# Optimization experiments

Hardware: AMD Instinct MI355X
Metric: run time of the kernel (lower is better)

Reference implementation:

```python
import jax, jax.numpy as jnp
import numpy as np

N = 50000
E = 1600000
F_IN = 128
C_OUT = 64
HEADS = 2
NEG_SLOPE = 0.2
EPS = 1e-5


def setup_inputs() -> dict:
    key = jax.random.key(0)
    ks = jax.random.split(key, 8)
    HC = HEADS * C_OUT
    glorot = lambda k, shape: jax.random.normal(k, shape, jnp.float32) * np.sqrt(2.0 / (shape[0] + shape[-1]))
    return {
        "x": jax.random.normal(ks[0], (N, F_IN), jnp.float32),
        "edge_index": jax.random.randint(ks[1], (2, E), 0, N, jnp.int64),
        "W_l": glorot(ks[2], (F_IN, HC)),
        "W_r": glorot(ks[3], (F_IN, HC)),
        "att": glorot(ks[4], (HEADS, C_OUT)),
        "bias": jnp.zeros((HC,), jnp.float32),
        "gn_weight": jnp.ones((HC,), jnp.float32),
        "gn_bias": jnp.zeros((HC,), jnp.float32),
        "gn_mean_scale": jnp.ones((HC,), jnp.float32),
    }


def reference(x, edge_index, W_l, W_r, att, bias, gn_weight, gn_bias, gn_mean_scale):
    n = x.shape[0]
    # --- GATv2Conv (share_weights=False, concat=True, dropout=0) ---
    x_l = (x @ W_l).reshape(n, HEADS, C_OUT)  # source transform
    x_r = (x @ W_r).reshape(n, HEADS, C_OUT)  # target transform
    # add self loops
    loop = jnp.arange(n, dtype=edge_index.dtype)
    src = jnp.concatenate([edge_index[0], loop])
    dst = jnp.concatenate([edge_index[1], loop])
    # edge-wise attention logits: LeakyReLU(x_l[j] + x_r[i]) . att
    xs = x_l[src] + x_r[dst]  # [E', H, C]
    e = jax.nn.leaky_relu(xs, NEG_SLOPE)
    logits = jnp.einsum('ehc,hc->eh', e, att)  # [E', H]
    # segment softmax over edges sharing the same target node
    seg_max = jax.ops.segment_max(logits, dst, num_segments=n)  # [N, H]
    exp = jnp.exp(logits - seg_max[dst])
    seg_sum = jax.ops.segment_sum(exp, dst, num_segments=n)
    alpha = exp / seg_sum[dst]  # [E', H]
    # scatter-aggregate messages
    msg = alpha[:, :, None] * x_l[src]  # [E', H, C]
    out = jax.ops.segment_sum(msg, dst, num_segments=n)  # [N, H, C]
    out = out.reshape(n, HEADS * C_OUT) + bias
    # --- GraphNorm (single graph) ---
    mean = out.mean(axis=0)
    centered = out - mean * gn_mean_scale
    var = (centered * centered).mean(axis=0)
    return gn_weight * centered / jnp.sqrt(var + EPS) + gn_bias
```

## Files before the change

kernel.cpp:

```cpp
#include <hip/hip_runtime.h>
#include <math.h>

#define NEG_SLOPE 0.2f
#define GN_EPS 1e-5f
#define NBSHIFT 8
#define CHUNK 2048

typedef _Float16 h2 __attribute__((ext_vector_type(2)));
typedef _Float16 half8 __attribute__((ext_vector_type(8)));
typedef float f32x4 __attribute__((ext_vector_type(4)));

__device__ __forceinline__ int rfl(int v) {
  return __builtin_amdgcn_readfirstlane(v);
}

__device__ __forceinline__ unsigned int pkh(float a, float b) {
  return __builtin_bit_cast(unsigned int, __builtin_amdgcn_cvt_pkrtz(a, b));
}

__device__ __forceinline__ h2 bch2(unsigned int u) {
  return __builtin_bit_cast(h2, u);
}

__device__ __forceinline__ h2 mkh2(float a, float b) {
  return __builtin_bit_cast(h2, __builtin_amdgcn_cvt_pkrtz(a, b));
}

__device__ __forceinline__ float dot2f(h2 a, h2 b, float c) {
#if __has_builtin(__builtin_amdgcn_fdot2)
  return __builtin_amdgcn_fdot2(a, b, c, false);
#else
  return fmaf((float)a.x, (float)b.x, fmaf((float)a.y, (float)b.y, c));
#endif
}

__device__ __forceinline__ float lkdot(h2 xl, h2 xr, h2 a, float p) {
  h2 t = xl + xr;
  h2 z = {(_Float16)0.f, (_Float16)0.f};
#if __has_builtin(__builtin_elementwise_min)
  h2 mn = __builtin_elementwise_min(t, z);
#else
  h2 mn;
  mn.x = (t.x < z.x) ? t.x : z.x;
  mn.y = (t.y < z.y) ? t.y : z.y;
#endif
  h2 km1 = {(_Float16)(NEG_SLOPE - 1.0f), (_Float16)(NEG_SLOPE - 1.0f)};
  h2 g = mn * km1 + t;
  return dot2f(g, a, p);
}

__global__ __launch_bounds__(256) void gemm_hist(
    const float* __restrict__ x, const float* __restrict__ Wl,
    const float* __restrict__ Wr, unsigned int* __restrict__ xlb,
    unsigned int* __restrict__ xrh, int n, const int* __restrict__ ei,
    int* __restrict__ bhist, int e, int gemm_blocks) {
  if ((int)blockIdx.x >= gemm_blocks) {
    __shared__ int hist[256];
    hist[threadIdx.x] = 0;
    __syncthreads();
    const int nbk = gridDim.x - gemm_blocks;
    const int stride = nbk * 256;
    for (int i = ((int)blockIdx.x - gemm_blocks) * 256 + threadIdx.x; i < e;
         i += stride)
      atomicAdd(&hist[ei[e + i] >> NBSHIFT], 1);
    __syncthreads();
    int v = hist[threadIdx.x];
    if (v > 0) atomicAdd(&bhist[threadIdx.x], v);
    return;
  }

  const int wv = threadIdx.x >> 6;
  const int lane = threadIdx.x & 63;
  const int lr = lane & 15;
  const int lk = lane >> 4;
  const int node0 = (int)blockIdx.x * 64;
  const float* __restrict__ Wp = (wv < 2) ? Wl : Wr;
  unsigned int* __restrict__ dst = (wv < 2) ? xlb : xrh;
  const int chBase = (wv & 1) * 64;

  f32x4 acc[4][4];
#pragma unroll
  for (int mt = 0; mt < 4; ++mt)
#pragma unroll
    for (int nt = 0; nt < 4; ++nt) acc[mt][nt] = (f32x4){0.f, 0.f, 0.f, 0.f};

  int nd[4];
#pragma unroll
  for (int nt = 0; nt < 4; ++nt) nd[nt] = min(node0 + nt * 16 + lr, n - 1);

#pragma unroll
  for (int kc = 0; kc < 4; ++kc) {
    const int k0 = kc * 32 + lk * 8;
    half8 a[4];
#pragma unroll
    for (int mt = 0; mt < 4; ++mt) {
      const float* __restrict__ wp =
          Wp + (size_t)k0 * 128 + chBase + mt * 16 + lr;
      float w0 = wp[0 * 128], w1 = wp[1 * 128], w2 = wp[2 * 128],
            w3 = wp[3 * 128];
      float w4 = wp[4 * 128], w5 = wp[5 * 128], w6 = wp[6 * 128],
            w7 = wp[7 * 128];
      uint4 ua;
      ua.x = pkh(w0, w1);
      ua.y = pkh(w2, w3);
      ua.z = pkh(w4, w5);
      ua.w = pkh(w6, w7);
      a[mt] = __builtin_bit_cast(half8, ua);
    }
    half8 b[4];
#pragma unroll
    for (int nt = 0; nt < 4; ++nt) {
      const float4 f0 = *(const float4*)(x + (size_t)nd[nt] * 128 + k0);
      const float4 f1 = *(const float4*)(x + (size_t)nd[nt] * 128 + k0 + 4);
      uint4 ub;
      ub.x = pkh(f0.x, f0.y);
      ub.y = pkh(f0.z, f0.w);
      ub.z = pkh(f1.x, f1.y);
      ub.w = pkh(f1.z, f1.w);
      b[nt] = __builtin_bit_cast(half8, ub);
    }
#pragma unroll
    for (int mt = 0; mt < 4; ++mt)
#pragma unroll
      for (int nt = 0; nt < 4; ++nt)
        acc[mt][nt] = __builtin_amdgcn_mfma_f32_16x16x32_f16(
            a[mt], b[nt], acc[mt][nt], 0, 0, 0);
  }

  const int dw0 = (chBase >> 1) + lk * 2;
#pragma unroll
  for (int nt = 0; nt < 4; ++nt) {
    const int node = node0 + nt * 16 + lr;
    if (node >= n) continue;
#pragma unroll
    for (int mt = 0; mt < 4; ++mt) {
      uint2 p;
      p.x = pkh(acc[mt][nt][0], acc[mt][nt][1]);
      p.y = pkh(acc[mt][nt][2], acc[mt][nt][3]);
      *(uint2*)(dst + (size_t)node * 64 + dw0 + mt * 8) = p;
    }
  }
}

__global__ __launch_bounds__(256) void bscan(const int* __restrict__ bhist,
                                             int* __restrict__ bbase,
                                             int* __restrict__ gcur,
                                             int* __restrict__ offsets, int nb,
                                             int n, int e) {
  __shared__ int sd[256];
  int t = threadIdx.x;
  int v = (t < nb) ? bhist[t] : 0;
  sd[t] = v;
  __syncthreads();
#pragma unroll
  for (int s = 1; s < 256; s <<= 1) {
    int add = (t >= s) ? sd[t - s] : 0;
    __syncthreads();
    sd[t] += add;
    __syncthreads();
  }
  int excl = sd[t] - v;
  if (t < nb) {
    bbase[t] = excl;
    gcur[t] = excl;
  } else {
    gcur[t] = 0;
  }
  if (t == 0) {
    bbase[nb] = e;
    offsets[n] = e;
  }
}

__global__ __launch_bounds__(256) void partition(const int* __restrict__ ei,
                                                 int* __restrict__ gcur,
                                                 unsigned int* __restrict__ ebuf,
                                                 int e) {
  __shared__ int hist[256];
  __shared__ int lcur[256];
  const int t = threadIdx.x;
  const int c0 = blockIdx.x * CHUNK;
  const int cend = min(c0 + CHUNK, e);
  hist[t] = 0;
  __syncthreads();
  for (int i = c0 + t; i < cend; i += 256)
    atomicAdd(&hist[ei[e + i] >> NBSHIFT], 1);
  __syncthreads();
  lcur[t] = atomicAdd(&gcur[t], hist[t]);
  __syncthreads();
  for (int i = c0 + t; i < cend; i += 256) {
    int dst = ei[e + i];
    int src = ei[i];
    int b = dst >> NBSHIFT;
    int pos = atomicAdd(&lcur[b], 1);
    ebuf[pos] = (unsigned int)src | ((unsigned int)(dst & 255) << 16);
  }
}

__global__ __launch_bounds__(1024) void csr_build(
    const unsigned int* __restrict__ ebuf, const int* __restrict__ bbase,
    int* __restrict__ offsets, int* __restrict__ csr_src, int n) {
  __shared__ int hist[256];
  __shared__ int sc[256];
  const int b = blockIdx.x;
  const int t = threadIdx.x;
  const int node0 = b << NBSHIFT;
  const int seg0 = bbase[b];
  const int seg1 = bbase[b + 1];

  if (t < 256) hist[t] = 0;
  __syncthreads();
  for (int i = seg0 + t; i < seg1; i += 1024)
    atomicAdd(&hist[(ebuf[i] >> 16) & 255], 1);
  __syncthreads();
  int v = 0;
  if (t < 256) {
    v = hist[t];
    sc[t] = v;
  }
  __syncthreads();
#pragma unroll
  for (int s = 1; s < 256; s <<= 1) {
    int add = (t >= s && t < 256) ? sc[t - s] : 0;
    __syncthreads();
    if (t < 256) sc[t] += add;
    __syncthreads();
  }
  if (t < 256) {
    int start = seg0 + sc[t] - v;
    int node = node0 + t;
    if (node < n) offsets[node] = start;
    hist[t] = start;
  }
  __syncthreads();
  for (int i = seg0 + t; i < seg1; i += 1024) {
    unsigned int u = ebuf[i];
    int pos = atomicAdd(&hist[(u >> 16) & 255], 1);
    csr_src[pos] = (int)(u & 0xFFFFu);
  }
}

__global__ __launch_bounds__(256) void node_agg(
    const unsigned int* __restrict__ xlh, const unsigned int* __restrict__ xrh,
    const int* __restrict__ offsets, const int* __restrict__ csr_src,
    const float* __restrict__ att, const float* __restrict__ bias,
    float* __restrict__ out, int n) {
  const int wave = threadIdx.x >> 6;
  const int lane = threadIdx.x & 63;
  const int node = blockIdx.x * 4 + wave;
  if (node >= n) return;
  const int q = lane >> 4;
  const int r = lane & 15;

  const uint4 xr4 = *(const uint4*)(xrh + (size_t)node * 64 + r * 4);
  const h2 xr0 = bch2(xr4.x), xr1 = bch2(xr4.y), xr2v = bch2(xr4.z),
           xr3 = bch2(xr4.w);
  const float4 a0 = *(const float4*)(att + r * 8);
  const float4 a1 = *(const float4*)(att + r * 8 + 4);
  const h2 ah0 = mkh2(a0.x, a0.y), ah1 = mkh2(a0.z, a0.w),
           ah2 = mkh2(a1.x, a1.y), ah3 = mkh2(a1.z, a1.w);

  const int start = rfl(offsets[node]);
  const int end = rfl(offsets[node + 1]);
  const int deg = end - start;
  const int T = deg + 1;

  float s = 0.f;
  float accf[8];
#pragma unroll
  for (int i = 0; i < 8; ++i) accf[i] = 0.f;

  const char* __restrict__ xlbase = (const char*)xlh;
  const unsigned roff = (unsigned)(r * 16);

  auto quad = [&](int src, bool valid) {
    const uint4 xl4 =
        *(const uint4*)(xlbase + (((unsigned)src << 8) | roff));
    const h2 x0 = bch2(xl4.x), x1 = bch2(xl4.y), x2 = bch2(xl4.z),
             x3 = bch2(xl4.w);
    float p = 0.f;
    p = lkdot(x0, xr0, ah0, p);
    p = lkdot(x1, xr1, ah1, p);
    p = lkdot(x2, xr2v, ah2, p);
    p = lkdot(x3, xr3, ah3, p);
    p += __shfl_xor(p, 1, 64);
    p += __shfl_xor(p, 2, 64);
    p += __shfl_xor(p, 4, 64);
    const float w = valid ? __expf(p) : 0.f;
    s += w;
    accf[0] = fmaf((float)x0.x, w, accf[0]);
    accf[1] = fmaf((float)x0.y, w, accf[1]);
    accf[2] = fmaf((float)x1.x, w, accf[2]);
    accf[3] = fmaf((float)x1.y, w, accf[3]);
    accf[4] = fmaf((float)x2.x, w, accf[4]);
    accf[5] = fmaf((float)x2.y, w, accf[5]);
    accf[6] = fmaf((float)x3.x, w, accf[6]);
    accf[7] = fmaf((float)x3.y, w, accf[7]);
  };

  for (int b0 = 0; b0 < T; b0 += 64) {
    const int m = min(64, T - b0);
    const int kk = b0 + lane;
    const int cl = min(kk, T - 1);
    int idx = node;
    if (deg > 0) {
      idx = csr_src[start + max(cl - 1, 0)];
      if (cl == 0) idx = node;
    }
    int j = 0;
#pragma unroll 2
    for (; j + 4 <= m; j += 4)
      quad(__shfl(idx, j + q, 64), true);
    if (j < m) {
      const int eo = j + q;
      quad(__shfl(idx, min(eo, m - 1), 64), eo < m);
    }
  }

  s += __shfl_xor(s, 16, 64);
  s += __shfl_xor(s, 32, 64);
#pragma unroll
  for (int i = 0; i < 8; ++i) {
    accf[i] += __shfl_xor(accf[i], 16, 64);
    accf[i] += __shfl_xor(accf[i], 32, 64);
  }

  if (q == 0) {
    const float inv = 1.f / s;
    const float4 b0v = *(const float4*)(bias + r * 8);
    const float4 b1v = *(const float4*)(bias + r * 8 + 4);
    float4 o0 = make_float4(fmaf(accf[0], inv, b0v.x), fmaf(accf[1], inv, b0v.y),
                            fmaf(accf[2], inv, b0v.z), fmaf(accf[3], inv, b0v.w));
    float4 o1 = make_float4(fmaf(accf[4], inv, b1v.x), fmaf(accf[5], inv, b1v.y),
                            fmaf(accf[6], inv, b1v.z), fmaf(accf[7], inv, b1v.w));
    *(float4*)(out + (size_t)node * 128 + r * 8) = o0;
    *(float4*)(out + (size_t)node * 128 + r * 8 + 4) = o1;
  }
}

__global__ __launch_bounds__(256) void gn_partial(const float4* __restrict__ out4,
                                                  float* __restrict__ part,
                                                  int total4) {
  const int t = threadIdx.x;
  float s0 = 0.f, s1 = 0.f, s2 = 0.f, s3 = 0.f;
  float q0 = 0.f, q1 = 0.f, q2 = 0.f, q3 = 0.f;
  const int stride = gridDim.x * 256;
  for (int i = blockIdx.x * 256 + t; i < total4; i += stride) {
    float4 v = out4[i];
    s0 += v.x; q0 = fmaf(v.x, v.x, q0);
    s1 += v.y; q1 = fmaf(v.y, v.y, q1);
    s2 += v.z; q2 = fmaf(v.z, v.z, q2);
    s3 += v.w; q3 = fmaf(v.w, v.w, q3);
  }
  __shared__ float red[8][128];
  const int row = t >> 5;
  const int cb = (t & 31) * 4;
  *(float4*)&red[row][cb] = make_float4(s0, s1, s2, s3);
  __syncthreads();
  if (t < 128) {
    float S = 0.f;
#pragma unroll
    for (int r = 0; r < 8; ++r) S += red[r][t];
    part[blockIdx.x * 256 + t] = S;
  }
  __syncthreads();
  *(float4*)&red[row][cb] = make_float4(q0, q1, q2, q3);
  __syncthreads();
  if (t < 128) {
    float Q = 0.f;
#pragma unroll
    for (int r = 0; r < 8; ++r) Q += red[r][t];
    part[blockIdx.x * 256 + 128 + t] = Q;
  }
}

__global__ __launch_bounds__(1024) void gn_final(const float* __restrict__ part,
                                                 const float* __restrict__ gw,
                                                 const float* __restrict__ gb,
                                                 const float* __restrict__ gms,
                                                 float* __restrict__ AB,
                                                 int nblocks, float inv_n) {
  __shared__ float sS[8][128];
  __shared__ float sQ[8][128];
  const int c = threadIdx.x & 127;
  const int sl = threadIdx.x >> 7;
  float S = 0.f, Q = 0.f;
#pragma unroll 8
  for (int b = sl; b < nblocks; b += 8) {
    S += part[b * 256 + c];
    Q += part[b * 256 + 128 + c];
  }
  sS[sl][c] = S;
  sQ[sl][c] = Q;
  __syncthreads();
  if (sl == 0) {
#pragma unroll
    for (int i = 1; i < 8; ++i) {
      S += sS[i][c];
      Q += sQ[i][c];
    }
    float mean = S * inv_n;
    float msc = mean * gms[c];
    float var = Q * inv_n - 2.f * msc * mean + msc * msc;
    float scale = gw[c] * rsqrtf(var + GN_EPS);
    AB[c] = scale;
    AB[128 + c] = gb[c] - scale * msc;
  }
}

__global__ void gn_apply(float* __restrict__ out, const float* __restrict__ AB,
                         int total4) {
  int i = blockIdx.x * blockDim.x + threadIdx.x;
  if (i >= total4) return;
  float4 v = ((float4*)out)[i];
  int c4 = (i & 31) * 4;
  v.x = fmaf(AB[c4 + 0], v.x, AB[128 + c4 + 0]);
  v.y = fmaf(AB[c4 + 1], v.y, AB[128 + c4 + 1]);
  v.z = fmaf(AB[c4 + 2], v.z, AB[128 + c4 + 2]);
  v.w = fmaf(AB[c4 + 3], v.w, AB[128 + c4 + 3]);
  ((float4*)out)[i] = v;
}

extern "C" void kernel_launch(void* const* d_in, const int* in_sizes, int n_in,
                              void* d_out, int out_size, void* d_ws,
                              size_t ws_size, hipStream_t stream) {
  const float* x = (const float*)d_in[0];
  const int* ei = (const int*)d_in[1];
  const float* Wl = (const float*)d_in[2];
  const float* Wr = (const float*)d_in[3];
  const float* att = (const float*)d_in[4];
  const float* bias = (const float*)d_in[5];
  const float* gw = (const float*)d_in[6];
  const float* gb = (const float*)d_in[7];
  const float* gms = (const float*)d_in[8];
  float* out = (float*)d_out;

  const int n = in_sizes[0] / 128;
  const int e = in_sizes[1] / 2;
  const int nb = (n + 255) >> NBSHIFT;
  const int nchunks = (e + CHUNK - 1) / CHUNK;
  const int GN_BLOCKS = 512;
  const int gemm_blocks = (n + 63) / 64;
  const int hist_blocks = 196;

  char* w = (char*)d_ws;
  auto alloc = [&](size_t bytes) {
    char* p = w;
    w += (bytes + 255) & ~(size_t)255;
    return p;
  };
  unsigned int* xlb = (unsigned int*)alloc((size_t)n * 64 * sizeof(int));
  unsigned int* xrh = (unsigned int*)alloc((size_t)n * 64 * sizeof(int));
  int* offsets = (int*)alloc((size_t)(n + 1) * sizeof(int));
  int* csr_src = (int*)alloc((size_t)e * sizeof(int));
  unsigned int* ebuf = (unsigned int*)alloc((size_t)e * sizeof(int));
  int* bhist = (int*)alloc(256 * sizeof(int));
  int* bbase = (int*)alloc((size_t)(nb + 1) * sizeof(int));
  int* gcur = (int*)alloc(256 * sizeof(int));
  float* part = (float*)alloc((size_t)GN_BLOCKS * 256 * sizeof(float));
  float* AB = (float*)alloc(256 * sizeof(float));

  hipMemsetAsync(bhist, 0, 256 * sizeof(int), stream);

  gemm_hist<<<gemm_blocks + hist_blocks, 256, 0, stream>>>(
      x, Wl, Wr, xlb, xrh, n, ei, bhist, e, gemm_blocks);
  bscan<<<1, 256, 0, stream>>>(bhist, bbase, gcur, offsets, nb, n, e);
  partition<<<nchunks, 256, 0, stream>>>(ei, gcur, ebuf, e);
  csr_build<<<nb, 1024, 0, stream>>>(ebuf, bbase, offsets, csr_src, n);
  node_agg<<<(n + 3) / 4, 256, 0, stream>>>(xlb, xrh, offsets, csr_src, att,
                                            bias, out, n);
  gn_partial<<<GN_BLOCKS, 256, 0, stream>>>((const float4*)out, part, n * 32);
  gn_final<<<1, 1024, 0, stream>>>(part, gw, gb, gms, AB, GN_BLOCKS,
                                   1.0f / (float)n);
  gn_apply<<<(n * 32 + 255) / 256, 256, 0, stream>>>(out, AB, n * 32);
}
```

Measured before the change: 241.3 us.

## Fuse GraphNorm statistics into node aggregation with atomics; use ds_swizzle reductions

Per-block column sums and sums of squares are now computed inside node_agg from values still in registers, reduced in shared memory and atomically added into a global 256-float accumulator. This removes the separate gn_partial pass that re-read the full output and shrinks gn_final. The intra-row shuffles become ds_swizzle calls and the edge loop unroll rises from 2 to 4. In exchange there are 12500 blocks each issuing 256 float atomics to the same addresses, which can contend and makes the summation order nondeterministic.

```diff
diff --git a/kernel.cpp b/kernel.cpp
--- a/kernel.cpp
+++ b/kernel.cpp
@@ -12,6 +12,13 @@
 
 __device__ __forceinline__ int rfl(int v) {
   return __builtin_amdgcn_readfirstlane(v);
+}
+
+template <int PAT>
+__device__ __forceinline__ float swz(float v) {
+  return __builtin_bit_cast(
+      float, (unsigned)__builtin_amdgcn_ds_swizzle(__builtin_bit_cast(int, v),
+                                                   PAT));
 }
 
 __device__ __forceinline__ unsigned int pkh(float a, float b) {
@@ -244,15 +251,18 @@
     const unsigned int* __restrict__ xlh, const unsigned int* __restrict__ xrh,
     const int* __restrict__ offsets, const int* __restrict__ csr_src,
     const float* __restrict__ att, const float* __restrict__ bias,
-    float* __restrict__ out, int n) {
+    float* __restrict__ out, float* __restrict__ SQ, int n) {
+  __shared__ float blkS[4][128];
+  __shared__ float blkQ[4][128];
   const int wave = threadIdx.x >> 6;
   const int lane = threadIdx.x & 63;
   const int node = blockIdx.x * 4 + wave;
-  if (node >= n) return;
+  const bool active = node < n;
+  const int nc = active ? node : 0;
   const int q = lane >> 4;
   const int r = lane & 15;
 
-  const uint4 xr4 = *(const uint4*)(xrh + (size_t)node * 64 + r * 4);
+  const uint4 xr4 = *(const uint4*)(xrh + (size_t)nc * 64 + r * 4);
   const h2 xr0 = bch2(xr4.x), xr1 = bch2(xr4.y), xr2v = bch2(xr4.z),
            xr3 = bch2(xr4.w);
   const float4 a0 = *(const float4*)(att + r * 8);
@@ -260,10 +270,10 @@
   const h2 ah0 = mkh2(a0.x, a0.y), ah1 = mkh2(a0.z, a0.w),
            ah2 = mkh2(a1.x, a1.y), ah3 = mkh2(a1.z, a1.w);
 
-  const int start = rfl(offsets[node]);
-  const int end = rfl(offsets[node + 1]);
+  const int start = rfl(offsets[nc]);
+  const int end = rfl(offsets[nc + 1]);
   const int deg = end - start;
-  const int T = deg + 1;
+  const int T = active ? deg + 1 : 0;
 
   float s = 0.f;
   float accf[8];
@@ -283,9 +293,9 @@
     p = lkdot(x1, xr1, ah1, p);
     p = lkdot(x2, xr2v, ah2, p);
     p = lkdot(x3, xr3, ah3, p);
-    p += __shfl_xor(p, 1, 64);
-    p += __shfl_xor(p, 2, 64);
-    p += __shfl_xor(p, 4, 64);
+    p += swz<0x041F>(p);
+    p += swz<0x081F>(p);
+    p += swz<0x101F>(p);
     const float w = valid ? __expf(p) : 0.f;
     s += w;
     accf[0] = fmaf((float)x0.x, w, accf[0]);
@@ -302,13 +312,13 @@
     const int m = min(64, T - b0);
     const int kk = b0 + lane;
     const int cl = min(kk, T - 1);
-    int idx = node;
+    int idx = nc;
     if (deg > 0) {
       idx = csr_src[start + max(cl - 1, 0)];
-      if (cl == 0) idx = node;
+      if (cl == 0) idx = nc;
     }
     int j = 0;
-#pragma unroll 2
+#pragma unroll 4
     for (; j + 4 <= m; j += 4)
       quad(__shfl(idx, j + q, 64), true);
     if (j < m) {
@@ -317,95 +327,60 @@
     }
   }
 
-  s += __shfl_xor(s, 16, 64);
+  s += swz<0x401F>(s);
   s += __shfl_xor(s, 32, 64);
 #pragma unroll
   for (int i = 0; i < 8; ++i) {
-    accf[i] += __shfl_xor(accf[i], 16, 64);
+    accf[i] += swz<0x401F>(accf[i]);
     accf[i] += __shfl_xor(accf[i], 32, 64);
   }
 
   if (q == 0) {
-    const float inv = 1.f / s;
-    const float4 b0v = *(const float4*)(bias + r * 8);
-    const float4 b1v = *(const float4*)(bias + r * 8 + 4);
-    float4 o0 = make_float4(fmaf(accf[0], inv, b0v.x), fmaf(accf[1], inv, b0v.y),
-                            fmaf(accf[2], inv, b0v.z), fmaf(accf[3], inv, b0v.w));
-    float4 o1 = make_float4(fmaf(accf[4], inv, b1v.x), fmaf(accf[5], inv, b1v.y),
-                            fmaf(accf[6], inv, b1v.z), fmaf(accf[7], inv, b1v.w));
-    *(float4*)(out + (size_t)node * 128 + r * 8) = o0;
-    *(float4*)(out + (size_t)node * 128 + r * 8 + 4) = o1;
-  }
-}
-
-__global__ __launch_bounds__(256) void gn_partial(const float4* __restrict__ out4,
-                                                  float* __restrict__ part,
-                                                  int total4) {
+    float4 o0 = make_float4(0.f, 0.f, 0.f, 0.f);
+    float4 o1 = make_float4(0.f, 0.f, 0.f, 0.f);
+    if (active) {
+      const float inv = 1.f / s;
+      const float4 b0v = *(const float4*)(bias + r * 8);
+      const float4 b1v = *(const float4*)(bias + r * 8 + 4);
+      o0 = make_float4(fmaf(accf[0], inv, b0v.x), fmaf(accf[1], inv, b0v.y),
+                       fmaf(accf[2], inv, b0v.z), fmaf(accf[3], inv, b0v.w));
+      o1 = make_float4(fmaf(accf[4], inv, b1v.x), fmaf(accf[5], inv, b1v.y),
+                       fmaf(accf[6], inv, b1v.z), fmaf(accf[7], inv, b1v.w));
+      *(float4*)(out + (size_t)node * 128 + r * 8) = o0;
+      *(float4*)(out + (size_t)node * 128 + r * 8 + 4) = o1;
+    }
+    *(float4*)&blkS[wave][r * 8] = o0;
+    *(float4*)&blkS[wave][r * 8 + 4] = o1;
+    float4 q0 = make_float4(o0.x * o0.x, o0.y * o0.y, o0.z * o0.z, o0.w * o0.w);
+    float4 q1 = make_float4(o1.x * o1.x, o1.y * o1.y, o1.z * o1.z, o1.w * o1.w);
+    *(float4*)&blkQ[wave][r * 8] = q0;
+    *(float4*)&blkQ[wave][r * 8 + 4] = q1;
+  }
+  __syncthreads();
   const int t = threadIdx.x;
-  float s0 = 0.f, s1 = 0.f, s2 = 0.f, s3 = 0.f;
-  float q0 = 0.f, q1 = 0.f, q2 = 0.f, q3 = 0.f;
-  const int stride = gridDim.x * 256;
-  for (int i = blockIdx.x * 256 + t; i < total4; i += stride) {
-    float4 v = out4[i];
-    s0 += v.x; q0 = fmaf(v.x, v.x, q0);
-    s1 += v.y; q1 = fmaf(v.y, v.y, q1);
-    s2 += v.z; q2 = fmaf(v.z, v.z, q2);
-    s3 += v.w; q3 = fmaf(v.w, v.w, q3);
-  }
-  __shared__ float red[8][128];
-  const int row = t >> 5;
-  const int cb = (t & 31) * 4;
-  *(float4*)&red[row][cb] = make_float4(s0, s1, s2, s3);
-  __syncthreads();
+  float v;
   if (t < 128) {
-    float S = 0.f;
-#pragma unroll
-    for (int r = 0; r < 8; ++r) S += red[r][t];
-    part[blockIdx.x * 256 + t] = S;
-  }
-  __syncthreads();
-  *(float4*)&red[row][cb] = make_float4(q0, q1, q2, q3);
-  __syncthreads();
-  if (t < 128) {
-    float Q = 0.f;
-#pragma unroll
-    for (int r = 0; r < 8; ++r) Q += red[r][t];
-    part[blockIdx.x * 256 + 128 + t] = Q;
-  }
-}
-
-__global__ __launch_bounds__(1024) void gn_final(const float* __restrict__ part,
-                                                 const float* __restrict__ gw,
-                                                 const float* __restrict__ gb,
-                                                 const float* __restrict__ gms,
-                                                 float* __restrict__ AB,
-                                                 int nblocks, float inv_n) {
-  __shared__ float sS[8][128];
-  __shared__ float sQ[8][128];
-  const int c = threadIdx.x & 127;
-  const int sl = threadIdx.x >> 7;
-  float S = 0.f, Q = 0.f;
-#pragma unroll 8
-  for (int b = sl; b < nblocks; b += 8) {
-    S += part[b * 256 + c];
-    Q += part[b * 256 + 128 + c];
-  }
-  sS[sl][c] = S;
-  sQ[sl][c] = Q;
-  __syncthreads();
-  if (sl == 0) {
-#pragma unroll
-    for (int i = 1; i < 8; ++i) {
-      S += sS[i][c];
-      Q += sQ[i][c];
-    }
-    float mean = S * inv_n;
-    float msc = mean * gms[c];
-    float var = Q * inv_n - 2.f * msc * mean + msc * msc;
-    float scale = gw[c] * rsqrtf(var + GN_EPS);
-    AB[c] = scale;
-    AB[128 + c] = gb[c] - scale * msc;
-  }
+    v = blkS[0][t] + blkS[1][t] + blkS[2][t] + blkS[3][t];
+  } else {
+    const int c = t - 128;
+    v = blkQ[0][c] + blkQ[1][c] + blkQ[2][c] + blkQ[3][c];
+  }
+  atomicAdd(&SQ[t], v);
+}
+
+__global__ void gn_final(const float* __restrict__ SQ,
+                         const float* __restrict__ gw,
+                         const float* __restrict__ gb,
+                         const float* __restrict__ gms, float* __restrict__ AB,
+                         float inv_n) {
+  int c = threadIdx.x;
+  float S = SQ[c], Q = SQ[128 + c];
+  float mean = S * inv_n;
+  float msc = mean * gms[c];
+  float var = Q * inv_n - 2.f * msc * mean + msc * msc;
+  float scale = gw[c] * rsqrtf(var + GN_EPS);
+  AB[c] = scale;
+  AB[128 + c] = gb[c] - scale * msc;
 }
 
 __global__ void gn_apply(float* __restrict__ out, const float* __restrict__ AB,
@@ -439,7 +414,6 @@
   const int e = in_sizes[1] / 2;
   const int nb = (n + 255) >> NBSHIFT;
   const int nchunks = (e + CHUNK - 1) / CHUNK;
-  const int GN_BLOCKS = 512;
   const int gemm_blocks = (n + 63) / 64;
   const int hist_blocks = 196;
 
@@ -455,12 +429,12 @@
   int* csr_src = (int*)alloc((size_t)e * sizeof(int));
   unsigned int* ebuf = (unsigned int*)alloc((size_t)e * sizeof(int));
   int* bhist = (int*)alloc(256 * sizeof(int));
+  float* SQ = (float*)alloc(256 * sizeof(float));
   int* bbase = (int*)alloc((size_t)(nb + 1) * sizeof(int));
   int* gcur = (int*)alloc(256 * sizeof(int));
-  float* part = (float*)alloc((size_t)GN_BLOCKS * 256 * sizeof(float));
   float* AB = (float*)alloc(256 * sizeof(float));
 
-  hipMemsetAsync(bhist, 0, 256 * sizeof(int), stream);
+  hipMemsetAsync(bhist, 0, 2048, stream);
 
   gemm_hist<<<gemm_blocks + hist_blocks, 256, 0, stream>>>(
       x, Wl, Wr, xlb, xrh, n, ei, bhist, e, gemm_blocks);
@@ -468,9 +442,7 @@
   partition<<<nchunks, 256, 0, stream>>>(ei, gcur, ebuf, e);
   csr_build<<<nb, 1024, 0, stream>>>(ebuf, bbase, offsets, csr_src, n);
   node_agg<<<(n + 3) / 4, 256, 0, stream>>>(xlb, xrh, offsets, csr_src, att,
-                                            bias, out, n);
-  gn_partial<<<GN_BLOCKS, 256, 0, stream>>>((const float4*)out, part, n * 32);
-  gn_final<<<1, 1024, 0, stream>>>(part, gw, gb, gms, AB, GN_BLOCKS,
-                                   1.0f / (float)n);
+                                            bias, out, SQ, n);
+  gn_final<<<1, 128, 0, stream>>>(SQ, gw, gb, gms, AB, 1.0f / (float)n);
   gn_apply<<<(n * 32 + 255) / 256, 256, 0, stream>>>(out, AB, n * 32);
 }
```

New measurement: 493.9 us. 105% more time.
